# Kernel tuning notes

Hardware: AMD Instinct MI355X
Metric: run time of the kernel (lower is better)

The kernel has to match this reference:

```python
import jax, jax.numpy as jnp
import numpy as np

EPS = 1e-5


def layer_norm(x, g, b):
    mu = jnp.mean(x, axis=-1, keepdims=True)
    var = jnp.mean((x - mu) ** 2, axis=-1, keepdims=True)
    return (x - mu) * jax.lax.rsqrt(var + EPS) * g + b


def rel_enc_shift(arr):
    # Transformer-XL shift trick: [b,n,l,m] -> shifted [b,n,l,m]
    b, n, l, m = arr.shape
    arr = jnp.concatenate([arr, jnp.zeros((b, n, l, 1), arr.dtype)], axis=-1)
    arr = arr.reshape(b, n, -1)
    arr = arr[:, :, l - 1:-1].reshape(b, n, l, m)
    return arr


def setup_inputs() -> dict:
    key = jax.random.key(0)
    B, S, M, D, H = 2, 1024, 1024, 1024, 16
    F = S + M
    ks = jax.random.split(key, 16)
    sc = 0.02
    inp = {
        "inputs": jax.random.normal(ks[0], (B, S, D), jnp.float32),
        "mem": jax.random.normal(ks[1], (B, M, D), jnp.float32),
        "rel_enc": jax.random.normal(ks[2], (F, D), jnp.float32),
        # causal mask with memory: query i may attend keys j <= i + M; 1 = masked
        "mask": (jnp.arange(F)[None, :] > (jnp.arange(S)[:, None] + M)).astype(jnp.float32)[None, None],
        "ln1_g": jnp.ones((D,), jnp.float32), "ln1_b": jnp.zeros((D,), jnp.float32),
        "wq": jax.random.normal(ks[3], (D, D), jnp.float32) * sc,
        "wke": jax.random.normal(ks[4], (D, D), jnp.float32) * sc,
        "wkr": jax.random.normal(ks[5], (D, D), jnp.float32) * sc,
        "wv": jax.random.normal(ks[6], (D, D), jnp.float32) * sc,
        "wf": jax.random.normal(ks[7], (D, D), jnp.float32) * sc,
        "u_param": jax.random.normal(ks[8], (1, 1, H, D // H), jnp.float32) * 0.05,
        "v_param": jax.random.normal(ks[9], (1, 1, H, D // H), jnp.float32) * 0.05,
        "ln2_g": jnp.ones((D,), jnp.float32), "ln2_b": jnp.zeros((D,), jnp.float32),
        "w1": jax.random.normal(ks[10], (D, D), jnp.float32) * sc,
        "b1": jnp.zeros((D,), jnp.float32),
        "w2": jax.random.normal(ks[11], (D, D), jnp.float32) * sc,
        "b2": jnp.zeros((D,), jnp.float32),
        "wg1": jax.random.normal(ks[12], (D, D), jnp.float32) * sc,
        "bg1": jnp.zeros((D,), jnp.float32),
        "wg2": jax.random.normal(ks[13], (D, D), jnp.float32) * sc,
        "bg2": jnp.zeros((D,), jnp.float32),
    }
    return inp


def _block(inputs, mem, mask, rel_enc, ln1_g, ln1_b, wq, wke, wkr, wv, wf,
           u_param, v_param, ln2_g, ln2_b, w1, b1, w2, b2, wg1, bg1, wg2, bg2):
    B, S, D = inputs.shape
    H = u_param.shape[2]
    dh = D // H
    x_tilde = jnp.concatenate([jax.lax.stop_gradient(mem), inputs], axis=1)
    F = x_tilde.shape[1]
    x_tilde = layer_norm(x_tilde, ln1_g, ln1_b)
    x = x_tilde[:, -S:, :]
    q = (x @ wq).reshape(B, S, H, dh)
    k = (x_tilde @ wke).reshape(B, F, H, dh)
    v = (x_tilde @ wv).reshape(B, F, H, dh)
    A_C = jnp.einsum('bsnd,bfnd->bnsf', q + u_param, k)
    Q = (rel_enc @ wkr).reshape(F, H, dh)
    B_D = rel_enc_shift(jnp.einsum('bsnd,fnd->bnsf', q + v_param, Q))
    score = (A_C + B_D) / jnp.sqrt(jnp.float32(D)) + mask * -1e10
    attn = jax.nn.softmax(score, axis=-1)
    attention_loss = jnp.mean(jnp.max(attn, axis=(-1, -2)))
    ao = jnp.einsum('bnsf,bfnd->bsnd', attn, v).reshape(B, S, D)
    rmha_out = jax.nn.gelu(ao @ wf, approximate=False)
    # gating 1 (output gating): x + sigmoid(Wx+b)*y
    g1 = inputs + jax.nn.sigmoid(inputs @ wg1 + bg1) * rmha_out
    h = layer_norm(g1, ln2_g, ln2_b)
    h = jax.nn.gelu(h @ w1 + b1, approximate=False)
    h = jax.nn.gelu(h @ w2 + b2, approximate=False)
    out = g1 + jax.nn.sigmoid(g1 @ wg2 + bg2) * h
    return out, attn, attention_loss


def reference(inputs, mem, mask, rel_enc, ln1_g, ln1_b, wq, wke, wkr, wv, wf,
              u_param, v_param, ln2_g, ln2_b, w1, b1, w2, b2, wg1, bg1, wg2, bg2):
    return _block(inputs, mem, mask, rel_enc, ln1_g, ln1_b, wq, wke, wkr, wv, wf,
                  u_param, v_param, ln2_g, ln2_b, w1, b1, w2, b2, wg1, bg1, wg2, bg2)
```

## Files before the change

### kernel.cpp

```cpp
#include <hip/hip_runtime.h>
#include <hip/hip_bf16.h>


typedef __attribute__((ext_vector_type(8))) short bf16x8;
typedef __attribute__((ext_vector_type(4))) float f32x4;

#define MFMA16(a, b, c) __builtin_amdgcn_mfma_f32_16x16x32_bf16((a), (b), (c), 0, 0, 0)

__device__ __forceinline__ unsigned short f2bf(float f) {
  union { __hip_bfloat16 h; unsigned short u; } cv;
  cv.h = __float2bfloat16(f);
  return cv.u;
}

__device__ __forceinline__ float bf2f(unsigned short u) {
  return __uint_as_float((unsigned)u << 16);
}

__device__ __forceinline__ float gelu_f(float x) {
  return 0.5f * x * (1.f + erff(x * 0.70710678118654752f));
}

struct W9 { const float* p[9]; };

__global__ __launch_bounds__(256) void k_init(
    const float* __restrict__ inputs, const float* __restrict__ mem,
    const float* __restrict__ rel_enc, const float* __restrict__ g1n,
    const float* __restrict__ b1n, W9 wp,
    unsigned short* __restrict__ xt, unsigned short* __restrict__ inb,
    unsigned short* __restrict__ reb, unsigned short* __restrict__ wT,
    float* __restrict__ amax) {
  int bid = blockIdx.x, tid = threadIdx.x;
  if (bid == 0 && tid < 32) amax[tid] = 0.f;
  if (bid < 4096) {
    __shared__ float red[8];
    int b = bid >> 11, fi = bid & 2047;
    const float* src = (fi < 1024)
        ? (mem + ((size_t)(b * 1024 + fi)) * 1024)
        : (inputs + ((size_t)(b * 1024 + fi - 1024)) * 1024);
    float4 x = ((const float4*)src)[tid];
    float s = x.x + x.y + x.z + x.w;
    float ss = x.x * x.x + x.y * x.y + x.z * x.z + x.w * x.w;
#pragma unroll
    for (int m = 32; m > 0; m >>= 1) {
      s += __shfl_down(s, m, 64);
      ss += __shfl_down(ss, m, 64);
    }
    int w = tid >> 6;
    if ((tid & 63) == 0) { red[w] = s; red[4 + w] = ss; }
    __syncthreads();
    s = red[0] + red[1] + red[2] + red[3];
    ss = red[4] + red[5] + red[6] + red[7];
    float mu = s * (1.f / 1024.f);
    float inv = rsqrtf(ss * (1.f / 1024.f) - mu * mu + 1e-5f);
    float4 g = ((const float4*)g1n)[tid];
    float4 bb = ((const float4*)b1n)[tid];
    ushort4 o;
    o.x = f2bf((x.x - mu) * inv * g.x + bb.x);
    o.y = f2bf((x.y - mu) * inv * g.y + bb.y);
    o.z = f2bf((x.z - mu) * inv * g.z + bb.z);
    o.w = f2bf((x.w - mu) * inv * g.w + bb.w);
    ((ushort4*)(xt + (size_t)bid * 1024))[tid] = o;
    if (fi >= 1024) {
      ushort4 r4;
      r4.x = f2bf(x.x); r4.y = f2bf(x.y); r4.z = f2bf(x.z); r4.w = f2bf(x.w);
      ((ushort4*)(inb + ((size_t)(b * 1024 + fi - 1024)) * 1024))[tid] = r4;
    }
  } else if (bid < 6144) {
    int r = bid - 4096;
    float4 x = ((const float4*)(rel_enc + (size_t)r * 1024))[tid];
    ushort4 o;
    o.x = f2bf(x.x); o.y = f2bf(x.y); o.z = f2bf(x.z); o.w = f2bf(x.w);
    ((ushort4*)(reb + (size_t)r * 1024))[tid] = o;
  } else {
    __shared__ float tl[64][65];
    int idx = bid - 6144;
    int m = idx >> 8;
    int t = idx & 255;
    int k0 = (t >> 4) << 6, n0 = (t & 15) << 6;
    const float* srcw = wp.p[m];
    int kr = tid >> 4, nc = (tid & 15) << 2;
#pragma unroll
    for (int i = 0; i < 4; ++i) {
      int krow = i * 16 + kr;
      float4 v = *(const float4*)(srcw + (size_t)(k0 + krow) * 1024 + n0 + nc);
      tl[nc + 0][krow] = v.x;
      tl[nc + 1][krow] = v.y;
      tl[nc + 2][krow] = v.z;
      tl[nc + 3][krow] = v.w;
    }
    __syncthreads();
    int n = tid >> 2, kc0 = (tid & 3) << 4;
    unsigned short* dst = wT + ((size_t)m << 20) + (size_t)(n0 + n) * 1024 + k0 + kc0;
#pragma unroll
    for (int q = 0; q < 4; ++q) {
      ushort4 o;
      o.x = f2bf(tl[n][kc0 + q * 4 + 0]);
      o.y = f2bf(tl[n][kc0 + q * 4 + 1]);
      o.z = f2bf(tl[n][kc0 + q * 4 + 2]);
      o.w = f2bf(tl[n][kc0 + q * 4 + 3]);
      *(ushort4*)(dst + q * 4) = o;
    }
  }
}

__global__ __launch_bounds__(256) void k_ln(
    const float* __restrict__ xin, const float* __restrict__ g1n,
    const float* __restrict__ b1n, unsigned short* __restrict__ outb) {
  __shared__ float red[8];
  int bid = blockIdx.x, tid = threadIdx.x;
  const float* src = xin + (size_t)bid * 1024;
  float4 x = ((const float4*)src)[tid];
  float s = x.x + x.y + x.z + x.w;
  float ss = x.x * x.x + x.y * x.y + x.z * x.z + x.w * x.w;
#pragma unroll
  for (int m = 32; m > 0; m >>= 1) {
    s += __shfl_down(s, m, 64);
    ss += __shfl_down(ss, m, 64);
  }
  int w = tid >> 6;
  if ((tid & 63) == 0) { red[w] = s; red[4 + w] = ss; }
  __syncthreads();
  s = red[0] + red[1] + red[2] + red[3];
  ss = red[4] + red[5] + red[6] + red[7];
  float mu = s * (1.f / 1024.f);
  float inv = rsqrtf(ss * (1.f / 1024.f) - mu * mu + 1e-5f);
  float4 g = ((const float4*)g1n)[tid];
  float4 bb = ((const float4*)b1n)[tid];
  ushort4 o;
  o.x = f2bf((x.x - mu) * inv * g.x + bb.x);
  o.y = f2bf((x.y - mu) * inv * g.y + bb.y);
  o.z = f2bf((x.z - mu) * inv * g.z + bb.z);
  o.w = f2bf((x.w - mu) * inv * g.w + bb.w);
  ((ushort4*)(outb + (size_t)bid * 1024))[tid] = o;
}

__device__ __forceinline__ int lds_u128(int r, int g) {
  return g * 128 + (r & ~7) + ((r ^ g) & 7);
}
template <int TM>
__device__ __forceinline__ int lds_uT(int r, int g) {
  return g * TM + (r & ~7) + ((r ^ g) & 7);
}

enum { EP_KV = 0, EP_QUV, EP_BF16, EP_GELU_F32, EP_GATE1,
       EP_GELU_B_BF16, EP_GELU_B_F32, EP_GATE2 };

template <int EP, int TM>
__global__ __launch_bounds__(256, 2) void k_gemm(
    const unsigned short* __restrict__ A, const unsigned short* __restrict__ Bw,
    int arow_add, int arow_mul,
    const float* __restrict__ bias, const float* __restrict__ auxA,
    const float* __restrict__ auxB, void* __restrict__ out0,
    void* __restrict__ out1) {
  constexpr int MI = TM / 16;
  constexpr int AU = TM / 32;
  __shared__ __align__(16) unsigned short As[2][TM * 64];
  __shared__ __align__(16) unsigned short Bs[2][128 * 64];
  int tid = threadIdx.x;
  int lane = tid & 63, wave = tid >> 6;
  int quad = lane >> 4, col = lane & 15;
  int bm = blockIdx.y, bn = blockIdx.x;
  f32x4 acc[MI][2] = {};
  int str = tid >> 3, stg = tid & 7;
  const unsigned short* aptr[AU];
  int au[AU];
  const unsigned short* bptr[4];
  int bu[4];
#pragma unroll
  for (int i = 0; i < AU; ++i) {
    int r = str + 32 * i;
    int gr = bm * TM + r;
    int ar = gr + arow_add + (gr >> 10) * arow_mul;
    aptr[i] = A + (size_t)ar * 1024 + stg * 8;
    au[i] = lds_uT<TM>(r, stg);
  }
#pragma unroll
  for (int i = 0; i < 4; ++i) {
    int r = str + 32 * i;
    bptr[i] = Bw + (size_t)(bn * 128 + r) * 1024 + stg * 8;
    bu[i] = lds_u128(r, stg);
  }
  uint4 av[AU], bv[4];
#pragma unroll
  for (int i = 0; i < AU; ++i) av[i] = *(const uint4*)(aptr[i]);
#pragma unroll
  for (int i = 0; i < 4; ++i) bv[i] = *(const uint4*)(bptr[i]);
#pragma unroll
  for (int i = 0; i < AU; ++i) ((uint4*)As[0])[au[i]] = av[i];
#pragma unroll
  for (int i = 0; i < 4; ++i) ((uint4*)Bs[0])[bu[i]] = bv[i];
  for (int kt = 0; kt < 16; ++kt) {
    __syncthreads();
    if (kt < 15) {
      int k0 = (kt + 1) * 64;
#pragma unroll
      for (int i = 0; i < AU; ++i) av[i] = *(const uint4*)(aptr[i] + k0);
#pragma unroll
      for (int i = 0; i < 4; ++i) bv[i] = *(const uint4*)(bptr[i] + k0);
    }
    int cur = kt & 1;
#pragma unroll
    for (int ks = 0; ks < 2; ++ks) {
      bf16x8 af[MI], bfr[2];
#pragma unroll
      for (int mi = 0; mi < MI; ++mi)
        af[mi] = ((const bf16x8*)As[cur])[lds_uT<TM>(mi * 16 + col, ks * 4 + quad)];
#pragma unroll
      for (int ni = 0; ni < 2; ++ni)
        bfr[ni] = ((const bf16x8*)Bs[cur])[lds_u128(wave * 32 + ni * 16 + col, ks * 4 + quad)];
#pragma unroll
      for (int mi = 0; mi < MI; ++mi)
#pragma unroll
        for (int ni = 0; ni < 2; ++ni)
          acc[mi][ni] = MFMA16(af[mi], bfr[ni], acc[mi][ni]);
    }
    if (kt < 15) {
      int nxt = cur ^ 1;
#pragma unroll
      for (int i = 0; i < AU; ++i) ((uint4*)As[nxt])[au[i]] = av[i];
#pragma unroll
      for (int i = 0; i < 4; ++i) ((uint4*)Bs[nxt])[bu[i]] = bv[i];
    }
  }
#pragma unroll
  for (int mi = 0; mi < MI; ++mi)
#pragma unroll
    for (int ni = 0; ni < 2; ++ni)
#pragma unroll
      for (int r = 0; r < 4; ++r) {
        int grow = bm * TM + mi * 16 + quad * 4 + r;
        int gcol = bn * 128 + wave * 32 + ni * 16 + col;
        float v = acc[mi][ni][r];
        size_t idx = (size_t)grow * 1024 + gcol;
        if constexpr (EP == EP_KV) {
          if (gcol < 1024) {
            ((unsigned short*)out0)[(size_t)grow * 1024 + gcol] = f2bf(v);
          } else {
            ((unsigned short*)out1)[(size_t)grow * 1024 + gcol - 1024] = f2bf(v);
          }
        } else if constexpr (EP == EP_QUV) {
          ((unsigned short*)out0)[idx] = f2bf(v + auxA[gcol]);
          ((unsigned short*)out1)[idx] = f2bf(v + auxB[gcol]);
        } else if constexpr (EP == EP_BF16) {
          ((unsigned short*)out0)[idx] = f2bf(v);
        } else if constexpr (EP == EP_GELU_F32) {
          ((float*)out0)[idx] = gelu_f(v);
        } else if constexpr (EP == EP_GATE1) {
          float a = v + bias[gcol];
          float sg = 1.f / (1.f + __expf(-a));
          float g1 = auxA[idx] + sg * auxB[idx];
          ((float*)out0)[idx] = g1;
          ((unsigned short*)out1)[idx] = f2bf(g1);
        } else if constexpr (EP == EP_GELU_B_BF16) {
          ((unsigned short*)out0)[idx] = f2bf(gelu_f(v + bias[gcol]));
        } else if constexpr (EP == EP_GELU_B_F32) {
          ((float*)out0)[idx] = gelu_f(v + bias[gcol]);
        } else {
          float a = v + bias[gcol];
          float sg = 1.f / (1.f + __expf(-a));
          ((float*)out0)[idx] = auxA[idx] + sg * auxB[idx];
        }
      }
}

__global__ __launch_bounds__(256) void k_tr(
    const unsigned short* __restrict__ v, unsigned short* __restrict__ vT) {
  __shared__ unsigned short tl[64][72];
  int bh = blockIdx.x, ft = blockIdx.y;
  int b = bh >> 4, h = bh & 15;
  int f0 = ft * 64;
  int tid = threadIdx.x;
  int fr = tid >> 2, c0 = (tid & 3) * 16;
  *(uint4*)&tl[fr][c0] =
      *(const uint4*)(v + ((size_t)(b * 2048 + f0 + fr)) * 1024 + h * 64 + c0);
  __syncthreads();
  int dr = tid >> 2, fc = (tid & 3) * 16;
  unsigned short* dst =
      vT + (((size_t)(b * 16 + h) * 64 + dr)) * 2048 + f0 + fc;
#pragma unroll
  for (int q = 0; q < 4; ++q) {
    ushort4 o;
    o.x = tl[fc + q * 4 + 0][dr];
    o.y = tl[fc + q * 4 + 1][dr];
    o.z = tl[fc + q * 4 + 2][dr];
    o.w = tl[fc + q * 4 + 3][dr];
    *(ushort4*)(dst + q * 4) = o;
  }
}

__global__ __launch_bounds__(256) void k_att(
    const unsigned short* __restrict__ qu, const unsigned short* __restrict__ qv,
    const unsigned short* __restrict__ kk, const unsigned short* __restrict__ vT,
    const unsigned short* __restrict__ Qr,
    float* __restrict__ attn, unsigned short* __restrict__ ao,
    float* __restrict__ amax) {
  __shared__ __align__(16) unsigned short Pb[16][2056];
  __shared__ __align__(16) float Ol[2][1024];
  __shared__ float Sl[4][16];
  __shared__ float Rinv[16];
  int tid = threadIdx.x, lane = tid & 63, wave = tid >> 6;
  int quad = lane >> 4, col = lane & 15;
  int bh = blockIdx.x, rt = blockIdx.y;
  int b = bh >> 4, h = bh & 15;
  int ri = rt * 16;

  bf16x8 quf[2], qvf[2];
  {
    const unsigned short* p0 = qu + ((size_t)(b * 1024 + ri + col)) * 1024 + h * 64 + quad * 8;
    quf[0] = *(const bf16x8*)p0;
    quf[1] = *(const bf16x8*)(p0 + 32);
    const unsigned short* p1 = qv + ((size_t)(b * 1024 + ri + col)) * 1024 + h * 64 + quad * 8;
    qvf[0] = *(const bf16x8*)p1;
    qvf[1] = *(const bf16x8*)(p1 + 32);
  }

  const unsigned short* qrbase = Qr + h * 64 + quad * 8;
  auto r_load = [&](int cbase, bf16x8& b0, bf16x8& b1) {
    int cr = cbase + col;
    cr = cr < 0 ? 0 : (cr > 2047 ? 2047 : cr);
    const unsigned short* p = qrbase + (size_t)cr * 1024;
    b0 = *(const bf16x8*)p;
    b1 = *(const bf16x8*)(p + 32);
  };
  auto r_mm = [&](bf16x8 b0, bf16x8 b1) -> f32x4 {
    f32x4 z = {0.f, 0.f, 0.f, 0.f};
    z = MFMA16(qvf[0], b0, z);
    z = MFMA16(qvf[1], b1, z);
    return z;
  };

  const unsigned short* kbase = kk + ((size_t)(b * 2048)) * 1024 + h * 64 + quad * 8;
  const unsigned short* vbase = vT + ((size_t)((b * 16 + h) * 64)) * 2048;

  f32x4 o4[4] = {};
  f32x4 srow = {0.f, 0.f, 0.f, 0.f};
  f32x4 pm = {0.f, 0.f, 0.f, 0.f};
  int jmax = ri + 15 + 1024;
  int jlo = wave * 512;

  if (jlo <= jmax) {
    int hi = jmax < jlo + 511 ? jmax : jlo + 511;
    int nch = ((hi - jlo) >> 5) + 1;
    int cw = 1008 - ri + jlo;
    f32x4 Rcur;
    {
      bf16x8 rb0, rb1;
      r_load(cw, rb0, rb1);
      Rcur = r_mm(rb0, rb1);
    }
    for (int ch = 0; ch < nch; ++ch) {
      int j0 = jlo + ch * 32;
      bf16x8 ra0, ra1, rc0, rc1;
      r_load(cw + 16, ra0, ra1);
      r_load(cw + 32, rc0, rc1);
      const unsigned short* kp0 = kbase + (size_t)(j0 + col) * 1024;
      const unsigned short* kp1 = kbase + (size_t)(j0 + 16 + col) * 1024;
      bf16x8 k00 = *(const bf16x8*)kp0;
      bf16x8 k01 = *(const bf16x8*)(kp0 + 32);
      bf16x8 k10 = *(const bf16x8*)kp1;
      bf16x8 k11 = *(const bf16x8*)(kp1 + 32);
      int fb = j0 + quad * 8;
      bf16x8 vf[4];
#pragma unroll
      for (int ni = 0; ni < 4; ++ni)
        vf[ni] = *(const bf16x8*)(vbase + (size_t)(ni * 16 + col) * 2048 + fb);
      f32x4 Rn1 = r_mm(ra0, ra1);
      f32x4 Rn2 = r_mm(rc0, rc1);
      f32x4 ac0 = {0.f, 0.f, 0.f, 0.f};
      ac0 = MFMA16(quf[0], k00, ac0);
      ac0 = MFMA16(quf[1], k01, ac0);
      f32x4 ac1 = {0.f, 0.f, 0.f, 0.f};
      ac1 = MFMA16(quf[0], k10, ac1);
      ac1 = MFMA16(quf[1], k11, ac1);
#pragma unroll
      for (int r = 0; r < 4; ++r) {
        int w = 15 + col - quad * 4 - r;
        int src = quad * 16 + (w & 15);
        float bd0 = __shfl(Rcur[r], src, 64);
        float bd1 = __shfl(Rn1[r], src, 64);
        float bd = (w < 16) ? bd0 : bd1;
        float sc = (ac0[r] + bd) * 0.03125f;
        int masked = (j0 + col) > (ri + quad * 4 + r + 1024);
        float p = masked ? 0.f : __expf(sc);
        srow[r] += p;
        pm[r] = fmaxf(pm[r], p);
        Pb[quad * 4 + r][j0 + col] = f2bf(p);
      }
#pragma unroll
      for (int r = 0; r < 4; ++r) {
        int w = 15 + col - quad * 4 - r;
        int src = quad * 16 + (w & 15);
        float bd0 = __shfl(Rn1[r], src, 64);
        float bd1 = __shfl(Rn2[r], src, 64);
        float bd = (w < 16) ? bd0 : bd1;
        float sc = (ac1[r] + bd) * 0.03125f;
        int masked = (j0 + 16 + col) > (ri + quad * 4 + r + 1024);
        float p = masked ? 0.f : __expf(sc);
        srow[r] += p;
        pm[r] = fmaxf(pm[r], p);
        Pb[quad * 4 + r][j0 + 16 + col] = f2bf(p);
      }
      asm volatile("s_waitcnt lgkmcnt(0)" ::: "memory");
      bf16x8 pf = *(const bf16x8*)&Pb[col][j0 + quad * 8];
#pragma unroll
      for (int ni = 0; ni < 4; ++ni) o4[ni] = MFMA16(pf, vf[ni], o4[ni]);
      Rcur = Rn2;
      cw += 32;
    }
  }
#pragma unroll
  for (int r = 0; r < 4; ++r) {
    float v = srow[r], m = pm[r];
    v += __shfl_xor(v, 1, 64);  m = fmaxf(m, __shfl_xor(m, 1, 64));
    v += __shfl_xor(v, 2, 64);  m = fmaxf(m, __shfl_xor(m, 2, 64));
    v += __shfl_xor(v, 4, 64);  m = fmaxf(m, __shfl_xor(m, 4, 64));
    v += __shfl_xor(v, 8, 64);  m = fmaxf(m, __shfl_xor(m, 8, 64));
    srow[r] = v; pm[r] = m;
  }
  if (col == 0) {
#pragma unroll
    for (int r = 0; r < 4; ++r) Sl[wave][quad * 4 + r] = srow[r];
  }
  if (wave >= 2) {
#pragma unroll
    for (int ni = 0; ni < 4; ++ni)
#pragma unroll
      for (int r = 0; r < 4; ++r)
        Ol[wave - 2][(quad * 4 + r) * 64 + ni * 16 + col] = o4[ni][r];
  }
  __syncthreads();
  if (tid < 16) {
    float rv = 1.f / (Sl[0][tid] + Sl[1][tid] + Sl[2][tid] + Sl[3][tid]);
    Rinv[tid] = rv;
  }
  if (wave < 2) {
#pragma unroll
    for (int ni = 0; ni < 4; ++ni)
#pragma unroll
      for (int r = 0; r < 4; ++r) {
        int ix = (quad * 4 + r) * 64 + ni * 16 + col;
        o4[ni][r] += Ol[wave][ix];
        if (wave == 1) Ol[1][ix] = o4[ni][r];
      }
  }
  __syncthreads();
  if (wave == 0) {
#pragma unroll
    for (int ni = 0; ni < 4; ++ni)
#pragma unroll
      for (int r = 0; r < 4; ++r) {
        int ix = (quad * 4 + r) * 64 + ni * 16 + col;
        o4[ni][r] += Ol[1][ix];
        Ol[0][ix] = o4[ni][r];
      }
  }
  __syncthreads();
  {
    int row = tid >> 4, d0 = (tid & 15) << 2;
    float4 ov = *(const float4*)&Ol[0][row * 64 + d0];
    float rv = Rinv[row];
    ushort4 o;
    o.x = f2bf(ov.x * rv); o.y = f2bf(ov.y * rv);
    o.z = f2bf(ov.z * rv); o.w = f2bf(ov.w * rv);
    *(ushort4*)(ao + ((size_t)(b * 1024 + ri + row)) * 1024 + h * 64 + d0) = o;
  }
  float pmax = 0.f;
#pragma unroll
  for (int r = 0; r < 4; ++r) pmax = fmaxf(pmax, pm[r] * Rinv[quad * 4 + r]);
  pmax = fmaxf(pmax, __shfl_xor(pmax, 16, 64));
  pmax = fmaxf(pmax, __shfl_xor(pmax, 32, 64));
  if (lane == 0) atomicMax((int*)(amax + bh), __float_as_int(pmax));

  {
    float* abase = attn + ((size_t)bh * 1024 + ri) * 2048;
#pragma unroll 4
    for (int it = 0; it < 32; ++it) {
      int idx = it * 256 + tid;
      int row = idx >> 9;
      int j = (idx & 511) << 2;
      float rv = Rinv[row];
      int lim = ri + row + 1024;
      ushort4 p4 = *(const ushort4*)&Pb[row][j];
      float4 o;
      o.x = (j + 0 <= lim) ? bf2f(p4.x) * rv : 0.f;
      o.y = (j + 1 <= lim) ? bf2f(p4.y) * rv : 0.f;
      o.z = (j + 2 <= lim) ? bf2f(p4.z) * rv : 0.f;
      o.w = (j + 3 <= lim) ? bf2f(p4.w) * rv : 0.f;
      *(float4*)(abase + (size_t)row * 2048 + j) = o;
    }
  }
}

__global__ void k_loss(const float* __restrict__ amax, float* __restrict__ out) {
  int l = threadIdx.x;
  float v = (l < 32) ? amax[l] : 0.f;
  v += __shfl_xor(v, 1, 64);
  v += __shfl_xor(v, 2, 64);
  v += __shfl_xor(v, 4, 64);
  v += __shfl_xor(v, 8, 64);
  v += __shfl_xor(v, 16, 64);
  v += __shfl_xor(v, 32, 64);
  if (l == 0) out[0] = v * (1.f / 32.f);
}

extern "C" void kernel_launch(void* const* d_in, const int* in_sizes, int n_in,
                              void* d_out, int out_size, void* d_ws, size_t ws_size,
                              hipStream_t stream) {
  (void)in_sizes; (void)n_in; (void)out_size; (void)ws_size;
  const float* inputs = (const float*)d_in[0];
  const float* mem    = (const float*)d_in[1];
  const float* rel    = (const float*)d_in[2];
  const float* ln1g   = (const float*)d_in[4];
  const float* ln1b   = (const float*)d_in[5];
  const float* wq     = (const float*)d_in[6];
  const float* wke    = (const float*)d_in[7];
  const float* wkr    = (const float*)d_in[8];
  const float* wv     = (const float*)d_in[9];
  const float* wf     = (const float*)d_in[10];
  const float* up     = (const float*)d_in[11];
  const float* vp     = (const float*)d_in[12];
  const float* ln2g   = (const float*)d_in[13];
  const float* ln2b   = (const float*)d_in[14];
  const float* w1     = (const float*)d_in[15];
  const float* b1     = (const float*)d_in[16];
  const float* w2     = (const float*)d_in[17];
  const float* b2     = (const float*)d_in[18];
  const float* wg1    = (const float*)d_in[19];
  const float* bg1    = (const float*)d_in[20];
  const float* wg2    = (const float*)d_in[21];
  const float* bg2    = (const float*)d_in[22];

  char* ws = (char*)d_ws;
  unsigned short* wT  = (unsigned short*)(ws);
  unsigned short* xt  = (unsigned short*)(ws + 18874368);
  unsigned short* inb = (unsigned short*)(ws + 27262976);
  unsigned short* reb = (unsigned short*)(ws + 31457280);
  unsigned short* kb  = (unsigned short*)(ws + 35651584);
  unsigned short* vTb = (unsigned short*)(ws + 44040192);
  unsigned short* qub = (unsigned short*)(ws + 52428800);
  unsigned short* qvb = (unsigned short*)(ws + 56623104);
  unsigned short* Qrb = (unsigned short*)(ws + 60817408);
  float* amax         = (float*)(ws + 65011712);
  unsigned short* vb = qub;
  float* rmha = (float*)xt;
  unsigned short* aob = reb;
  float* g1f = (float*)kb;
  float* h2f = (float*)vTb;
  unsigned short* g1b = qub;
  unsigned short* h0b = qvb;
  unsigned short* h1b = Qrb;

  float* outp  = (float*)d_out;
  float* attnp = outp + 2097152;
  float* lossp = outp + 69206016;

  W9 wp;
  wp.p[0] = wq;  wp.p[1] = wke; wp.p[2] = wv;  wp.p[3] = wkr; wp.p[4] = wf;
  wp.p[5] = w1;  wp.p[6] = w2;  wp.p[7] = wg1; wp.p[8] = wg2;

  k_init<<<8448, 256, 0, stream>>>(inputs, mem, rel, ln1g, ln1b, wp,
                                   xt, inb, reb, wT, amax);
  k_gemm<EP_KV, 64><<<dim3(16, 64), 256, 0, stream>>>(
      xt, wT + (1u << 20), 0, 0, nullptr, nullptr, nullptr, kb, vb);
  k_tr<<<dim3(32, 32), 256, 0, stream>>>(vb, vTb);
  k_gemm<EP_QUV, 32><<<dim3(8, 64), 256, 0, stream>>>(
      xt, wT, 1024, 1024, nullptr, up, vp, qub, qvb);
  k_gemm<EP_BF16, 32><<<dim3(8, 64), 256, 0, stream>>>(
      reb, wT + 3u * (1u << 20), 0, 0, nullptr, nullptr, nullptr, Qrb, nullptr);
  k_att<<<dim3(32, 64), 256, 0, stream>>>(qub, qvb, kb, vTb, Qrb,
                                          attnp, aob, amax);
  k_gemm<EP_GELU_F32, 32><<<dim3(8, 64), 256, 0, stream>>>(
      aob, wT + 4u * (1u << 20), 0, 0, nullptr, nullptr, nullptr, rmha, nullptr);
  k_gemm<EP_GATE1, 32><<<dim3(8, 64), 256, 0, stream>>>(
      inb, wT + 7u * (1u << 20), 0, 0, bg1, inputs, rmha, g1f, g1b);
  k_ln<<<2048, 256, 0, stream>>>(g1f, ln2g, ln2b, h0b);
  k_gemm<EP_GELU_B_BF16, 32><<<dim3(8, 64), 256, 0, stream>>>(
      h0b, wT + 5u * (1u << 20), 0, 0, b1, nullptr, nullptr, h1b, nullptr);
  k_gemm<EP_GELU_B_F32, 32><<<dim3(8, 64), 256, 0, stream>>>(
      h1b, wT + 6u * (1u << 20), 0, 0, b2, nullptr, nullptr, h2f, nullptr);
  k_gemm<EP_GATE2, 32><<<dim3(8, 64), 256, 0, stream>>>(
      g1b, wT + 8u * (1u << 20), 0, 0, bg2, g1f, h2f, outp, nullptr);
  k_loss<<<1, 64, 0, stream>>>(amax, lossp);
}
```

Before: 715.4 us.

## Interleave attention key chunks across waves and double-buffer chunk loads

```diff
diff --git a/kernel.cpp b/kernel.cpp
--- a/kernel.cpp
+++ b/kernel.cpp
@@ -289,7 +289,7 @@
   }
 }
 
-__global__ __launch_bounds__(256) void k_att(
+__global__ __launch_bounds__(256, 2) void k_att(
     const unsigned short* __restrict__ qu, const unsigned short* __restrict__ qv,
     const unsigned short* __restrict__ kk, const unsigned short* __restrict__ vT,
     const unsigned short* __restrict__ Qr,
@@ -337,78 +337,87 @@
   f32x4 srow = {0.f, 0.f, 0.f, 0.f};
   f32x4 pm = {0.f, 0.f, 0.f, 0.f};
   int jmax = ri + 15 + 1024;
-  int jlo = wave * 512;
-
-  if (jlo <= jmax) {
-    int hi = jmax < jlo + 511 ? jmax : jlo + 511;
-    int nch = ((hi - jlo) >> 5) + 1;
-    int cw = 1008 - ri + jlo;
-    f32x4 Rcur;
-    {
-      bf16x8 rb0, rb1;
-      r_load(cw, rb0, rb1);
-      Rcur = r_mm(rb0, rb1);
-    }
-    for (int ch = 0; ch < nch; ++ch) {
-      int j0 = jlo + ch * 32;
-      bf16x8 ra0, ra1, rc0, rc1;
-      r_load(cw + 16, ra0, ra1);
-      r_load(cw + 32, rc0, rc1);
-      const unsigned short* kp0 = kbase + (size_t)(j0 + col) * 1024;
-      const unsigned short* kp1 = kbase + (size_t)(j0 + 16 + col) * 1024;
-      bf16x8 k00 = *(const bf16x8*)kp0;
-      bf16x8 k01 = *(const bf16x8*)(kp0 + 32);
-      bf16x8 k10 = *(const bf16x8*)kp1;
-      bf16x8 k11 = *(const bf16x8*)(kp1 + 32);
-      int fb = j0 + quad * 8;
-      bf16x8 vf[4];
-#pragma unroll
-      for (int ni = 0; ni < 4; ++ni)
-        vf[ni] = *(const bf16x8*)(vbase + (size_t)(ni * 16 + col) * 2048 + fb);
-      f32x4 Rn1 = r_mm(ra0, ra1);
-      f32x4 Rn2 = r_mm(rc0, rc1);
-      f32x4 ac0 = {0.f, 0.f, 0.f, 0.f};
-      ac0 = MFMA16(quf[0], k00, ac0);
-      ac0 = MFMA16(quf[1], k01, ac0);
-      f32x4 ac1 = {0.f, 0.f, 0.f, 0.f};
-      ac1 = MFMA16(quf[0], k10, ac1);
-      ac1 = MFMA16(quf[1], k11, ac1);
-#pragma unroll
-      for (int r = 0; r < 4; ++r) {
-        int w = 15 + col - quad * 4 - r;
-        int src = quad * 16 + (w & 15);
-        float bd0 = __shfl(Rcur[r], src, 64);
-        float bd1 = __shfl(Rn1[r], src, 64);
-        float bd = (w < 16) ? bd0 : bd1;
-        float sc = (ac0[r] + bd) * 0.03125f;
-        int masked = (j0 + col) > (ri + quad * 4 + r + 1024);
-        float p = masked ? 0.f : __expf(sc);
-        srow[r] += p;
-        pm[r] = fmaxf(pm[r], p);
-        Pb[quad * 4 + r][j0 + col] = f2bf(p);
-      }
-#pragma unroll
-      for (int r = 0; r < 4; ++r) {
-        int w = 15 + col - quad * 4 - r;
-        int src = quad * 16 + (w & 15);
-        float bd0 = __shfl(Rn1[r], src, 64);
-        float bd1 = __shfl(Rn2[r], src, 64);
-        float bd = (w < 16) ? bd0 : bd1;
-        float sc = (ac1[r] + bd) * 0.03125f;
-        int masked = (j0 + 16 + col) > (ri + quad * 4 + r + 1024);
-        float p = masked ? 0.f : __expf(sc);
-        srow[r] += p;
-        pm[r] = fmaxf(pm[r], p);
-        Pb[quad * 4 + r][j0 + 16 + col] = f2bf(p);
-      }
-      asm volatile("s_waitcnt lgkmcnt(0)" ::: "memory");
-      bf16x8 pf = *(const bf16x8*)&Pb[col][j0 + quad * 8];
-#pragma unroll
-      for (int ni = 0; ni < 4; ++ni) o4[ni] = MFMA16(pf, vf[ni], o4[ni]);
-      Rcur = Rn2;
-      cw += 32;
-    }
-  }
+  int NA = (jmax >> 5) + 1;
+  int myN = (NA - wave + 3) >> 2;
+
+  auto load_chunk = [&](int j0, int cw, bf16x8* rr, bf16x8* kr, bf16x8* vr) {
+    r_load(cw, rr[0], rr[1]);
+    r_load(cw + 16, rr[2], rr[3]);
+    r_load(cw + 32, rr[4], rr[5]);
+    const unsigned short* kp0 = kbase + (size_t)(j0 + col) * 1024;
+    const unsigned short* kp1 = kbase + (size_t)(j0 + 16 + col) * 1024;
+    kr[0] = *(const bf16x8*)kp0;
+    kr[1] = *(const bf16x8*)(kp0 + 32);
+    kr[2] = *(const bf16x8*)kp1;
+    kr[3] = *(const bf16x8*)(kp1 + 32);
+    int fb = j0 + quad * 8;
+#pragma unroll
+    for (int ni = 0; ni < 4; ++ni)
+      vr[ni] = *(const bf16x8*)(vbase + (size_t)(ni * 16 + col) * 2048 + fb);
+  };
+
+  auto compute_chunk = [&](int j0, bf16x8* rr, bf16x8* kr, bf16x8* vr) {
+    f32x4 R0 = r_mm(rr[0], rr[1]);
+    f32x4 R1 = r_mm(rr[2], rr[3]);
+    f32x4 R2 = r_mm(rr[4], rr[5]);
+    f32x4 ac0 = {0.f, 0.f, 0.f, 0.f};
+    ac0 = MFMA16(quf[0], kr[0], ac0);
+    ac0 = MFMA16(quf[1], kr[1], ac0);
+    f32x4 ac1 = {0.f, 0.f, 0.f, 0.f};
+    ac1 = MFMA16(quf[0], kr[2], ac1);
+    ac1 = MFMA16(quf[1], kr[3], ac1);
+#pragma unroll
+    for (int r = 0; r < 4; ++r) {
+      int w = 15 + col - quad * 4 - r;
+      int src = quad * 16 + (w & 15);
+      float bd0 = __shfl(R0[r], src, 64);
+      float bd1 = __shfl(R1[r], src, 64);
+      float bd = (w < 16) ? bd0 : bd1;
+      float sc = (ac0[r] + bd) * 0.03125f;
+      int masked = (j0 + col) > (ri + quad * 4 + r + 1024);
+      float p = masked ? 0.f : __expf(sc);
+      srow[r] += p;
+      pm[r] = fmaxf(pm[r], p);
+      Pb[quad * 4 + r][j0 + col] = f2bf(p);
+    }
+#pragma unroll
+    for (int r = 0; r < 4; ++r) {
+      int w = 15 + col - quad * 4 - r;
+      int src = quad * 16 + (w & 15);
+      float bd0 = __shfl(R1[r], src, 64);
+      float bd1 = __shfl(R2[r], src, 64);
+      float bd = (w < 16) ? bd0 : bd1;
+      float sc = (ac1[r] + bd) * 0.03125f;
+      int masked = (j0 + 16 + col) > (ri + quad * 4 + r + 1024);
+      float p = masked ? 0.f : __expf(sc);
+      srow[r] += p;
+      pm[r] = fmaxf(pm[r], p);
+      Pb[quad * 4 + r][j0 + 16 + col] = f2bf(p);
+    }
+    asm volatile("s_waitcnt lgkmcnt(0)" ::: "memory");
+    bf16x8 pf = *(const bf16x8*)&Pb[col][j0 + quad * 8];
+#pragma unroll
+    for (int ni = 0; ni < 4; ++ni) o4[ni] = MFMA16(pf, vr[ni], o4[ni]);
+  };
+
+  {
+    bf16x8 Ar[6], Ak[4], Av[4], Br[6], Bk[4], Bv[4];
+    int j0 = wave << 5;
+    int cw = 1008 - ri + j0;
+    load_chunk(j0, cw, Ar, Ak, Av);
+    int i = 0;
+    while (true) {
+      if (i + 1 < myN) load_chunk(j0 + 128, cw + 128, Br, Bk, Bv);
+      compute_chunk(j0, Ar, Ak, Av);
+      ++i; j0 += 128; cw += 128;
+      if (i >= myN) break;
+      if (i + 1 < myN) load_chunk(j0 + 128, cw + 128, Ar, Ak, Av);
+      compute_chunk(j0, Br, Bk, Bv);
+      ++i; j0 += 128; cw += 128;
+      if (i >= myN) break;
+    }
+  }
+
 #pragma unroll
   for (int r = 0; r < 4; ++r) {
     float v = srow[r], m = pm[r];
```

New measurement: 709.0 us. Within noise of the previous version (-0.9%).
